# Kernel optimization log

Hardware: AMD Instinct MI355X
Metric: run time of the kernel (lower is better)

Reference implementation:

```python
import jax, jax.numpy as jnp
import numpy as np

N, CIO, L = 16, 512, 384
DIMHEAD, NUMHEAD, MAXEMBED, DIMGROUP = 64, 8, 384, 8
CHID = DIMHEAD * NUMHEAD


def setup_inputs() -> dict:
    key = jax.random.key(0)
    ks = jax.random.split(key, 12)
    s = 0.05
    return {
        "x": jax.random.normal(ks[0], (N, CIO, L), jnp.float32),
        "xorg": jax.random.normal(ks[1], (N, CIO, L), jnp.float32),
        "abspos": jax.random.normal(ks[2], (N, CIO, L), jnp.float32),
        "mask": jnp.zeros((N, L), jnp.float32),
        "norm": jnp.full((N,), 8.0, jnp.float32),
        "qkpos_res": s * jax.random.normal(ks[3], (CIO // DIMGROUP, 1), jnp.float32),
        "qkorg_res": s * jax.random.normal(ks[4], (CIO // DIMGROUP, 1), jnp.float32),
        "vorg_res": s * jax.random.normal(ks[5], (CIO // DIMGROUP, 1), jnp.float32),
        "relpos": s * jax.random.normal(ks[6], (2 * MAXEMBED - 1,), jnp.float32),
        "gate_w": s * jax.random.normal(ks[7], (NUMHEAD, CIO), jnp.float32),
        "gate_b": jnp.zeros((NUMHEAD,), jnp.float32),
        "q_w": s * jax.random.normal(ks[8], (CHID, CIO), jnp.float32),
        "k_w": s * jax.random.normal(ks[9], (CHID, CIO), jnp.float32),
        "v_w": s * jax.random.normal(ks[10], (CHID, CIO), jnp.float32),
        "dense_w": s * jax.random.normal(ks[11], (CIO, CHID), jnp.float32),
        "dense_b": jnp.zeros((CIO,), jnp.float32),
    }


def _rezero(t, res):
    # (N,C,L) -> reshape to (N, C//DIMGROUP, DIMGROUP*L), scale per group, reshape back
    n, c, l = t.shape
    return (t.reshape(n, c // DIMGROUP, -1) * res).reshape(n, c, l)


def _relpos_idx():
    # idx[i, j] = clip(MAXEMBED - i + j, 0, 2*MAXEMBED - 2)
    idx = np.arange(MAXEMBED, MAXEMBED - L, -1)[:, None] + np.arange(L)[None, :]
    return jnp.asarray(np.clip(idx, 0, 2 * MAXEMBED - 2))


def reference(x, xorg, abspos, mask, norm, qkpos_res, qkorg_res, vorg_res,
              relpos, gate_w, gate_b, q_w, k_w, v_w, dense_w, dense_b):
    n = x.shape[0]
    x0 = x + _rezero(xorg, vorg_res)                     # value path
    x1 = x + _rezero(xorg, qkorg_res) + _rezero(abspos, qkpos_res)  # qk path

    q = jnp.einsum('oc,ncl->nol', q_w, x1).reshape(n, NUMHEAD, DIMHEAD, L)
    k = jnp.einsum('oc,ncl->nol', k_w, x1).reshape(n, NUMHEAD, DIMHEAD, L)
    v = jnp.einsum('oc,ncl->nol', v_w, x0).reshape(n, NUMHEAD, DIMHEAD, L)

    scores = jnp.einsum('nhdi,nhdj->nhij', q, k)         # (N, H, L, L)
    gate = jnp.einsum('oc,ncl->nol', gate_w, x) + gate_b[None, :, None]  # (N, H, L)
    scores = (scores + relpos[_relpos_idx()]
              + gate[:, :, None, :]
              + mask[:, None, None, :]) / norm[:, None, None, None]

    attn = jax.nn.softmax(scores, axis=-1)
    out = jnp.einsum('nhij,nhdj->nhdi', attn, v).reshape(n, CHID, L)
    out = jnp.einsum('oc,ncl->nol', dense_w, out) + dense_b[None, :, None]
    return out
```

## Files before the change

kernel.cpp:

```cpp
#include <hip/hip_runtime.h>
#include <hip/hip_bf16.h>

#define N_B   16
#define CIO   512
#define LSEQ  384
#define DH    64
#define NH    8
#define CHID  512
#define ME    384

typedef __hip_bfloat16 bf16;
typedef __attribute__((ext_vector_type(8))) short bf16x8;
typedef __attribute__((ext_vector_type(4))) float f32x4;

#define AS1 __attribute__((address_space(1)))
#define AS3 __attribute__((address_space(3)))

__device__ __forceinline__ unsigned short f2bs(float f) {
    union { bf16 b; unsigned short u; } cv; cv.b = __float2bfloat16(f); return cv.u;
}

__device__ __forceinline__ void gload_lds16(const bf16* g, bf16* l) {
    __builtin_amdgcn_global_load_lds((const AS1 unsigned int*)g,
                                     (AS3 unsigned int*)l, 16, 0, 0);
}

__launch_bounds__(256)
__global__ void prep_kernel(const float* __restrict__ x, const float* __restrict__ xorg,
                            const float* __restrict__ abspos,
                            const float* __restrict__ qkorg, const float* __restrict__ qkpos,
                            const float* __restrict__ vorg,
                            const float* __restrict__ gw,
                            const float* __restrict__ q_w, const float* __restrict__ k_w,
                            const float* __restrict__ v_w, const float* __restrict__ dense_w,
                            bf16* __restrict__ wqb, bf16* __restrict__ wkb,
                            bf16* __restrict__ wvb, bf16* __restrict__ wdb,
                            bf16* __restrict__ x1t, bf16* __restrict__ x0t,
                            float* __restrict__ gpart)
{
    __shared__ bf16 T1[64 * 72], T0[64 * 72];
    __shared__ float Traw[64 * 65];
    __shared__ float gws[NH * 64];
    __shared__ float r0[64], r1[64], r2[64];
    const int tid = threadIdx.x;
    const int cb = blockIdx.x;
    const int c0 = cb * 64;
    const int l0 = blockIdx.y * 64;
    const int n  = blockIdx.z;

    {
        int f = blockIdx.x + 8 * (blockIdx.y + 6 * blockIdx.z);
        if (f < 512) {
            int e = (f * 256 + tid) * 8;
            int which = e >> 18;
            int off = e & ((1 << 18) - 1);
            const float* s = which == 0 ? q_w : which == 1 ? k_w : which == 2 ? v_w : dense_w;
            bf16* d       = which == 0 ? wqb : which == 1 ? wkb : which == 2 ? wvb : wdb;
            float4 f0 = *(const float4*)&s[off];
            float4 f1 = *(const float4*)&s[off + 4];
            unsigned short u[8] = {f2bs(f0.x), f2bs(f0.y), f2bs(f0.z), f2bs(f0.w),
                                   f2bs(f1.x), f2bs(f1.y), f2bs(f1.z), f2bs(f1.w)};
            *(uint4*)&d[off] = *(uint4*)u;
        }
    }

    if (tid < 64) {
        int gidx = (c0 + tid) >> 3;
        r0[tid] = vorg[gidx];
        r1[tid] = qkorg[gidx];
        r2[tid] = qkpos[gidx];
    }
    for (int t = tid; t < NH * 64; t += 256) {
        int h = t >> 6, c = t & 63;
        gws[t] = gw[h * CIO + c0 + c];
    }
    __syncthreads();
    const int l = tid & 63, cs = tid >> 6;
    #pragma unroll
    for (int r = 0; r < 16; r++) {
        int cl = r * 4 + cs;
        size_t gi = ((size_t)n * CIO + c0 + cl) * LSEQ + l0 + l;
        float xv = x[gi], xo = xorg[gi];
        Traw[cl * 65 + l] = xv;
        T0[l * 72 + cl] = __float2bfloat16(xv + r0[cl] * xo);
        T1[l * 72 + cl] = __float2bfloat16(xv + r1[cl] * xo + r2[cl] * abspos[gi]);
    }
    __syncthreads();
    for (int t = tid; t < NH * 64; t += 256) {
        int h = t >> 6, ll = t & 63;
        float s = 0.f;
        #pragma unroll
        for (int c = 0; c < 64; c++) s += gws[h * 64 + c] * Traw[c * 65 + ll];
        gpart[(((size_t)cb * N_B + n) * NH + h) * LSEQ + l0 + ll] = s;
    }
    #pragma unroll
    for (int t = 0; t < 2; t++) {
        int idx = t * 256 + tid;
        int lr = idx >> 3, u = idx & 7;
        size_t go = ((size_t)n * LSEQ + l0 + lr) * CIO + c0 + u * 8;
        *(uint4*)&x1t[go] = *(const uint4*)&T1[lr * 72 + u * 8];
        *(uint4*)&x0t[go] = *(const uint4*)&T0[lr * 72 + u * 8];
    }
}

__launch_bounds__(256)
__global__ void qkv_kernel(const bf16* __restrict__ wall,
                           const bf16* __restrict__ x1t, const bf16* __restrict__ x0t,
                           bf16* __restrict__ qb, bf16* __restrict__ kb,
                           bf16* __restrict__ vb)
{
    __shared__ __align__(16) char smem[17408];
    bf16* As = (bf16*)smem;
    bf16* Bs = (bf16*)(smem + 8192);
    bf16* S  = (bf16*)smem;

    const int tid = threadIdx.x;
    const int lane = tid & 63, w = tid >> 6;
    const int l15 = lane & 15, g = lane >> 4;
    const int Bid = blockIdx.x;
    const int rres = Bid & 7, qq = Bid >> 3;
    const int n = rres + 8 * (qq / 36);
    const int t = qq % 36;
    const int ot = t / 3;
    const int lt = t % 3;
    const int osub = (w & 1) * 64, lsub = (w >> 1) * 64;

    const bf16* Wt = wall + (size_t)(ot * 128) * CIO;
    const bf16* Bt = (ot < 8 ? x1t : x0t) + ((size_t)n * LSEQ + lt * 128) * CIO;

    const int segA = 2 * w, segB = 2 * w + 1;
    const int eA = segA * 512 + lane * 8;
    const int eB = segB * 512 + lane * 8;
    const int rA = eA >> 5, cA = eA & 31;
    const int rB = eB >> 5, cB = eB & 31;

    f32x4 acc[4][4];
    #pragma unroll
    for (int mt = 0; mt < 4; mt++)
        #pragma unroll
        for (int jt = 0; jt < 4; jt++) acc[mt][jt] = f32x4{0.f, 0.f, 0.f, 0.f};

    for (int it = 0; it < 16; ++it) {
        const int k0 = it * 32;
        gload_lds16(Wt + (size_t)rA * CIO + k0 + cA, As + segA * 512);
        gload_lds16(Wt + (size_t)rB * CIO + k0 + cB, As + segB * 512);
        gload_lds16(Bt + (size_t)rA * CIO + k0 + cA, Bs + segA * 512);
        gload_lds16(Bt + (size_t)rB * CIO + k0 + cB, Bs + segB * 512);
        __syncthreads();
        bf16x8 af[4], bfv[4];
        #pragma unroll
        for (int mt = 0; mt < 4; mt++)
            af[mt] = *(const bf16x8*)&As[(osub + mt * 16 + l15) * 32 + 8 * g];
        #pragma unroll
        for (int jt = 0; jt < 4; jt++)
            bfv[jt] = *(const bf16x8*)&Bs[(lsub + jt * 16 + l15) * 32 + 8 * g];
        #pragma unroll
        for (int mt = 0; mt < 4; mt++)
            #pragma unroll
            for (int jt = 0; jt < 4; jt++)
                acc[mt][jt] = __builtin_amdgcn_mfma_f32_16x16x32_bf16(af[mt], bfv[jt], acc[mt][jt], 0, 0, 0);
        __syncthreads();
    }

    if (ot < 8) {
        bf16* dstb = (ot < 4) ? qb : kb;
        const int hbase = 2 * (ot & 3);
        #pragma unroll
        for (int lh = 0; lh < 2; ++lh) {
            if ((w >> 1) == lh) {
                #pragma unroll
                for (int mt = 0; mt < 4; mt++)
                    #pragma unroll
                    for (int jt = 0; jt < 4; jt++)
                        #pragma unroll
                        for (int r = 0; r < 4; r++)
                            S[(jt * 16 + l15) * 136 + osub + mt * 16 + 4 * g + r] =
                                __float2bfloat16(acc[mt][jt][r]);
            }
            __syncthreads();
            #pragma unroll
            for (int t2 = 0; t2 < 4; ++t2) {
                int idx = t2 * 256 + tid;
                int lr = idx >> 4, u = idx & 15;
                int ho = u >> 3, dc = u & 7;
                bf16* dst = dstb + (((size_t)n * NH + hbase + ho) * LSEQ
                                    + lt * 128 + lh * 64 + lr) * DH + dc * 8;
                *(uint4*)dst = *(const uint4*)&S[lr * 136 + u * 8];
            }
            __syncthreads();
        }
    } else {
        const int ob = (ot - 8) * 128;
        #pragma unroll
        for (int oh = 0; oh < 2; ++oh) {
            if ((w & 1) == oh) {
                #pragma unroll
                for (int mt = 0; mt < 4; mt++)
                    #pragma unroll
                    for (int jt = 0; jt < 4; jt++)
                        #pragma unroll
                        for (int r = 0; r < 4; r++)
                            S[(mt * 16 + 4 * g + r) * 136 + lsub + jt * 16 + l15] =
                                __float2bfloat16(acc[mt][jt][r]);
            }
            __syncthreads();
            #pragma unroll
            for (int t2 = 0; t2 < 4; ++t2) {
                int idx = t2 * 256 + tid;
                int orr = idx >> 4, u = idx & 15;
                bf16* dst = vb + ((size_t)(n * CHID + ob + oh * 64 + orr)) * LSEQ
                               + lt * 128 + u * 8;
                *(uint4*)dst = *(const uint4*)&S[orr * 136 + u * 8];
            }
            __syncthreads();
        }
    }
}

__launch_bounds__(256, 3)
__global__ void attn_kernel(const bf16* __restrict__ qt,
                            const bf16* __restrict__ kt,
                            const bf16* __restrict__ v,
                            const float* __restrict__ gpart,
                            const float* __restrict__ gb,
                            const float* __restrict__ mask,
                            const float* __restrict__ norm,
                            const float* __restrict__ relpos,
                            bf16* __restrict__ ctxt)
{
    __shared__ __align__(16) char smem[25600];
    __shared__ float relp_s[2 * ME - 1];
    __shared__ float radd_s[LSEQ];

    bf16* P = (bf16*)smem;
    bf16* O = (bf16*)smem;

    const int tid = threadIdx.x;
    const int Bid = blockIdx.x;
    const int rres = Bid & 7, qq = Bid >> 3;
    const int n = rres + 8 * (qq / 48);
    const int rem = qq % 48;
    const int h = rem / 6;
    const int i0 = (rem % 6) * 64;
    const int lane = tid & 63;
    const int w = tid >> 6;
    const int l15 = lane & 15, g = lane >> 4;
    const int m0 = w * 16;

    const size_t nh = (size_t)n * NH + h;
    const bf16* kt_g = kt + nh * LSEQ * DH;
    const bf16* vg   = v + ((size_t)n * CHID + h * DH) * LSEQ;

    {
        const float gbh = gb[h];
        for (int i = tid; i < LSEQ; i += 256) {
            float s = gbh + mask[(size_t)n * LSEQ + i];
            #pragma unroll
            for (int cb = 0; cb < 8; cb++)
                s += gpart[(((size_t)cb * N_B + n) * NH + h) * LSEQ + i];
            radd_s[i] = s;
        }
    }
    for (int i = tid; i < 2 * ME - 1; i += 256) relp_s[i] = relpos[i];

    const bf16* qrow = qt + (nh * LSEQ + i0 + m0 + l15) * DH;
    bf16x8 a0 = *(const bf16x8*)&qrow[8 * g];
    bf16x8 a1 = *(const bf16x8*)&qrow[8 * g + 32];
    const float inv_norm = 1.0f / norm[n];
    __syncthreads();

    f32x4 acc[24];
    #pragma unroll
    for (int jt = 0; jt < 24; jt++) acc[jt] = f32x4{0.f, 0.f, 0.f, 0.f};
    #pragma unroll
    for (int jt = 0; jt < 24; jt++) {
        const bf16* kr = &kt_g[(size_t)(jt * 16 + l15) * DH + 8 * g];
        bf16x8 b0 = *(const bf16x8*)kr;
        bf16x8 b1 = *(const bf16x8*)(kr + 32);
        acc[jt] = __builtin_amdgcn_mfma_f32_16x16x32_bf16(a0, b0, acc[jt], 0, 0, 0);
        acc[jt] = __builtin_amdgcn_mfma_f32_16x16x32_bf16(a1, b1, acc[jt], 0, 0, 0);
    }

    const int ib = i0 + m0 + 4 * g;
    float mx[4] = {-1e30f, -1e30f, -1e30f, -1e30f};
    #pragma unroll
    for (int jt = 0; jt < 24; jt++) {
        float ra = radd_s[jt * 16 + l15];
        #pragma unroll
        for (int r = 0; r < 4; r++) {
            int idx = ME - (ib + r) + jt * 16 + l15;
            idx = (idx > 2 * ME - 2) ? (2 * ME - 2) : idx;
            float s = (acc[jt][r] + relp_s[idx] + ra) * inv_norm;
            acc[jt][r] = s;
            mx[r] = fmaxf(mx[r], s);
        }
    }
    #pragma unroll
    for (int r = 0; r < 4; r++)
        #pragma unroll
        for (int off = 1; off <= 8; off <<= 1)
            mx[r] = fmaxf(mx[r], __shfl_xor(mx[r], off));
    float sm[4] = {0.f, 0.f, 0.f, 0.f};
    #pragma unroll
    for (int jt = 0; jt < 24; jt++) {
        #pragma unroll
        for (int r = 0; r < 4; r++) {
            float e = __expf(acc[jt][r] - mx[r]);
            acc[jt][r] = e;
            sm[r] += e;
        }
    }
    #pragma unroll
    for (int r = 0; r < 4; r++) {
        #pragma unroll
        for (int off = 1; off <= 8; off <<= 1)
            sm[r] += __shfl_xor(sm[r], off);
        sm[r] = 1.0f / sm[r];
    }

    f32x4 oacc[4];
    #pragma unroll
    for (int dn = 0; dn < 4; dn++) oacc[dn] = f32x4{0.f, 0.f, 0.f, 0.f};
    #pragma unroll
    for (int half = 0; half < 2; half++) {
        #pragma unroll
        for (int jt = 0; jt < 12; jt++)
            #pragma unroll
            for (int r = 0; r < 4; r++)
                P[(m0 + 4 * g + r) * 200 + jt * 16 + l15] =
                    __float2bfloat16(acc[half * 12 + jt][r] * sm[r]);
        bf16x8 vreg[2][4];
        #pragma unroll
        for (int dn = 0; dn < 4; dn++)
            vreg[0][dn] = *(const bf16x8*)&vg[(size_t)(dn * 16 + l15) * LSEQ + half * 192 + 8 * g];
        #pragma unroll
        for (int jt2 = 0; jt2 < 6; jt2++) {
            const int s = jt2 & 1;
            if (jt2 < 5) {
                #pragma unroll
                for (int dn = 0; dn < 4; dn++)
                    vreg[s ^ 1][dn] = *(const bf16x8*)&vg[(size_t)(dn * 16 + l15) * LSEQ + half * 192 + (jt2 + 1) * 32 + 8 * g];
            }
            bf16x8 a = *(const bf16x8*)&P[(m0 + l15) * 200 + jt2 * 32 + 8 * g];
            #pragma unroll
            for (int dn = 0; dn < 4; dn++)
                oacc[dn] = __builtin_amdgcn_mfma_f32_16x16x32_bf16(a, vreg[s][dn], oacc[dn], 0, 0, 0);
        }
    }

    __syncthreads();
    #pragma unroll
    for (int dn = 0; dn < 4; dn++)
        #pragma unroll
        for (int r = 0; r < 4; r++)
            O[(m0 + 4 * g + r) * 72 + dn * 16 + l15] = __float2bfloat16(oacc[dn][r]);
    __syncthreads();

    bf16* cg_ = ctxt + ((size_t)n * LSEQ + i0) * CHID + h * DH;
    #pragma unroll
    for (int t = 0; t < 2; t++) {
        int idx = t * 256 + tid;
        int ir = idx >> 3, u = idx & 7;
        *(uint4*)&cg_[(size_t)ir * CHID + u * 8] = *(const uint4*)&O[ir * 72 + u * 8];
    }
}

__launch_bounds__(256, 6)
__global__ void dense_kernel(const bf16* __restrict__ Wb,
                             const bf16* __restrict__ Bt,
                             const float* __restrict__ bias,
                             float* __restrict__ outf)
{
    __shared__ __align__(16) float S[64 * 68];
    const int tid = threadIdx.x;
    const int lane = tid & 63, w = tid >> 6;
    const int l15 = lane & 15, g = lane >> 4;
    const int Bid = blockIdx.x;
    const int rres = Bid & 7, qq = Bid >> 3;
    const int n = rres + 8 * (qq / 48);
    const int tt = qq % 48;
    const int o0 = (tt / 6) * 64;
    const int l0 = (tt % 6) * 64;

    const bf16* arow = Wb + (size_t)(o0 + l15) * CIO + 8 * g;
    const bf16* brow = Bt + ((size_t)n * LSEQ + l0 + w * 16 + l15) * CIO + 8 * g;

    f32x4 acc[4];
    #pragma unroll
    for (int mt = 0; mt < 4; mt++) acc[mt] = f32x4{0.f, 0.f, 0.f, 0.f};
    #pragma unroll 4
    for (int it = 0; it < 16; it++) {
        const int k0 = it * 32;
        bf16x8 b = *(const bf16x8*)&brow[k0];
        bf16x8 a[4];
        #pragma unroll
        for (int mt = 0; mt < 4; mt++)
            a[mt] = *(const bf16x8*)&arow[(size_t)mt * 16 * CIO + k0];
        #pragma unroll
        for (int mt = 0; mt < 4; mt++)
            acc[mt] = __builtin_amdgcn_mfma_f32_16x16x32_bf16(a[mt], b, acc[mt], 0, 0, 0);
    }

    #pragma unroll
    for (int mt = 0; mt < 4; mt++)
        #pragma unroll
        for (int r = 0; r < 4; r++)
            S[(mt * 16 + 4 * g + r) * 68 + w * 16 + l15] =
                acc[mt][r] + bias[o0 + mt * 16 + 4 * g + r];
    __syncthreads();
    float* og = outf + ((size_t)n * CHID + o0) * LSEQ + l0;
    #pragma unroll
    for (int t = 0; t < 4; t++) {
        int idx = t * 256 + tid;
        int orow = idx >> 4, u = idx & 15;
        *(float4*)&og[(size_t)orow * LSEQ + u * 4] = *(const float4*)&S[orow * 68 + u * 4];
    }
}

extern "C" void kernel_launch(void* const* d_in, const int* in_sizes, int n_in,
                              void* d_out, int out_size, void* d_ws, size_t ws_size,
                              hipStream_t stream)
{
    const float* x       = (const float*)d_in[0];
    const float* xorg    = (const float*)d_in[1];
    const float* abspos  = (const float*)d_in[2];
    const float* mask    = (const float*)d_in[3];
    const float* norm    = (const float*)d_in[4];
    const float* qkpos   = (const float*)d_in[5];
    const float* qkorg   = (const float*)d_in[6];
    const float* vorg    = (const float*)d_in[7];
    const float* relpos  = (const float*)d_in[8];
    const float* gate_w  = (const float*)d_in[9];
    const float* gate_b  = (const float*)d_in[10];
    const float* q_w     = (const float*)d_in[11];
    const float* k_w     = (const float*)d_in[12];
    const float* v_w     = (const float*)d_in[13];
    const float* dense_w = (const float*)d_in[14];
    const float* dense_b = (const float*)d_in[15];
    float* out = (float*)d_out;

    const size_t TEN = (size_t)N_B * CHID * LSEQ * sizeof(bf16);
    const size_t WB  = (size_t)CHID * CIO * sizeof(bf16);
    char* ws = (char*)d_ws;
    bf16*  x1t  = (bf16*)(ws);
    bf16*  x0t  = (bf16*)(ws + TEN);
    bf16*  qb   = (bf16*)(ws + 2 * TEN);
    bf16*  kb   = (bf16*)(ws + 3 * TEN);
    bf16*  vb   = (bf16*)(ws + 4 * TEN);
    bf16*  wqb  = (bf16*)(ws + 5 * TEN);
    bf16*  wkb  = (bf16*)(ws + 5 * TEN + WB);
    bf16*  wvb  = (bf16*)(ws + 5 * TEN + 2 * WB);
    bf16*  wdb  = (bf16*)(ws + 5 * TEN + 3 * WB);
    float* gpart = (float*)(ws + 5 * TEN + 4 * WB);
    bf16*  ctxt = x1t;

    prep_kernel<<<dim3(CIO / 64, LSEQ / 64, N_B), 256, 0, stream>>>(
        x, xorg, abspos, qkorg, qkpos, vorg, gate_w,
        q_w, k_w, v_w, dense_w, wqb, wkb, wvb, wdb, x1t, x0t, gpart);
    qkv_kernel<<<576, 256, 0, stream>>>(wqb, x1t, x0t, qb, kb, vb);
    attn_kernel<<<768, 256, 0, stream>>>(qb, kb, vb, gpart, gate_b,
                                         mask, norm, relpos, ctxt);
    dense_kernel<<<768, 256, 0, stream>>>(wdb, ctxt, dense_b, out);
}
```

Before: 199.4 us.

## Use online softmax over two key halves to cut score register footprint

```diff
diff --git a/kernel.cpp b/kernel.cpp
--- a/kernel.cpp
+++ b/kernel.cpp
@@ -269,77 +269,75 @@
     const float inv_norm = 1.0f / norm[n];
     __syncthreads();
 
-    f32x4 acc[24];
-    #pragma unroll
-    for (int jt = 0; jt < 24; jt++) acc[jt] = f32x4{0.f, 0.f, 0.f, 0.f};
-    #pragma unroll
-    for (int jt = 0; jt < 24; jt++) {
-        const bf16* kr = &kt_g[(size_t)(jt * 16 + l15) * DH + 8 * g];
-        bf16x8 b0 = *(const bf16x8*)kr;
-        bf16x8 b1 = *(const bf16x8*)(kr + 32);
-        acc[jt] = __builtin_amdgcn_mfma_f32_16x16x32_bf16(a0, b0, acc[jt], 0, 0, 0);
-        acc[jt] = __builtin_amdgcn_mfma_f32_16x16x32_bf16(a1, b1, acc[jt], 0, 0, 0);
-    }
-
     const int ib = i0 + m0 + 4 * g;
-    float mx[4] = {-1e30f, -1e30f, -1e30f, -1e30f};
-    #pragma unroll
-    for (int jt = 0; jt < 24; jt++) {
-        float ra = radd_s[jt * 16 + l15];
+    f32x4 oacc[4];
+    #pragma unroll
+    for (int dn = 0; dn < 4; dn++) oacc[dn] = f32x4{0.f, 0.f, 0.f, 0.f};
+    float m_r[4]  = {-1e30f, -1e30f, -1e30f, -1e30f};
+    float lsum[4] = {0.f, 0.f, 0.f, 0.f};
+
+    #pragma unroll
+    for (int half = 0; half < 2; half++) {
+        const int j0 = half * 192;
+
+        f32x4 acc[12];
+        #pragma unroll
+        for (int jt = 0; jt < 12; jt++) acc[jt] = f32x4{0.f, 0.f, 0.f, 0.f};
+        #pragma unroll
+        for (int jt = 0; jt < 12; jt++) {
+            const bf16* kr = &kt_g[(size_t)(j0 + jt * 16 + l15) * DH + 8 * g];
+            bf16x8 b0 = *(const bf16x8*)kr;
+            bf16x8 b1 = *(const bf16x8*)(kr + 32);
+            acc[jt] = __builtin_amdgcn_mfma_f32_16x16x32_bf16(a0, b0, acc[jt], 0, 0, 0);
+            acc[jt] = __builtin_amdgcn_mfma_f32_16x16x32_bf16(a1, b1, acc[jt], 0, 0, 0);
+        }
+
+        float mx[4] = {-1e30f, -1e30f, -1e30f, -1e30f};
+        #pragma unroll
+        for (int jt = 0; jt < 12; jt++) {
+            float ra = radd_s[j0 + jt * 16 + l15];
+            #pragma unroll
+            for (int r = 0; r < 4; r++) {
+                int idx = ME - (ib + r) + j0 + jt * 16 + l15;
+                idx = (idx > 2 * ME - 2) ? (2 * ME - 2) : idx;
+                float s = (acc[jt][r] + relp_s[idx] + ra) * inv_norm;
+                acc[jt][r] = s;
+                mx[r] = fmaxf(mx[r], s);
+            }
+        }
         #pragma unroll
         for (int r = 0; r < 4; r++) {
-            int idx = ME - (ib + r) + jt * 16 + l15;
-            idx = (idx > 2 * ME - 2) ? (2 * ME - 2) : idx;
-            float s = (acc[jt][r] + relp_s[idx] + ra) * inv_norm;
-            acc[jt][r] = s;
-            mx[r] = fmaxf(mx[r], s);
-        }
-    }
-    #pragma unroll
-    for (int r = 0; r < 4; r++)
-        #pragma unroll
-        for (int off = 1; off <= 8; off <<= 1)
-            mx[r] = fmaxf(mx[r], __shfl_xor(mx[r], off));
-    float sm[4] = {0.f, 0.f, 0.f, 0.f};
-    #pragma unroll
-    for (int jt = 0; jt < 24; jt++) {
-        #pragma unroll
-        for (int r = 0; r < 4; r++) {
-            float e = __expf(acc[jt][r] - mx[r]);
-            acc[jt][r] = e;
-            sm[r] += e;
-        }
-    }
-    #pragma unroll
-    for (int r = 0; r < 4; r++) {
-        #pragma unroll
-        for (int off = 1; off <= 8; off <<= 1)
-            sm[r] += __shfl_xor(sm[r], off);
-        sm[r] = 1.0f / sm[r];
-    }
-
-    f32x4 oacc[4];
-    #pragma unroll
-    for (int dn = 0; dn < 4; dn++) oacc[dn] = f32x4{0.f, 0.f, 0.f, 0.f};
-    #pragma unroll
-    for (int half = 0; half < 2; half++) {
-        #pragma unroll
-        for (int jt = 0; jt < 12; jt++)
-            #pragma unroll
-            for (int r = 0; r < 4; r++)
-                P[(m0 + 4 * g + r) * 200 + jt * 16 + l15] =
-                    __float2bfloat16(acc[half * 12 + jt][r] * sm[r]);
+            #pragma unroll
+            for (int off = 1; off <= 8; off <<= 1)
+                mx[r] = fmaxf(mx[r], __shfl_xor(mx[r], off));
+            float mnew = fmaxf(m_r[r], mx[r]);
+            float sc = __expf(m_r[r] - mnew);
+            m_r[r] = mnew;
+            lsum[r] *= sc;
+            #pragma unroll
+            for (int dn = 0; dn < 4; dn++) oacc[dn][r] *= sc;
+        }
+        #pragma unroll
+        for (int jt = 0; jt < 12; jt++) {
+            #pragma unroll
+            for (int r = 0; r < 4; r++) {
+                float e = __expf(acc[jt][r] - m_r[r]);
+                lsum[r] += e;
+                P[(m0 + 4 * g + r) * 200 + jt * 16 + l15] = __float2bfloat16(e);
+            }
+        }
+
         bf16x8 vreg[2][4];
         #pragma unroll
         for (int dn = 0; dn < 4; dn++)
-            vreg[0][dn] = *(const bf16x8*)&vg[(size_t)(dn * 16 + l15) * LSEQ + half * 192 + 8 * g];
+            vreg[0][dn] = *(const bf16x8*)&vg[(size_t)(dn * 16 + l15) * LSEQ + j0 + 8 * g];
         #pragma unroll
         for (int jt2 = 0; jt2 < 6; jt2++) {
             const int s = jt2 & 1;
             if (jt2 < 5) {
                 #pragma unroll
                 for (int dn = 0; dn < 4; dn++)
-                    vreg[s ^ 1][dn] = *(const bf16x8*)&vg[(size_t)(dn * 16 + l15) * LSEQ + half * 192 + (jt2 + 1) * 32 + 8 * g];
+                    vreg[s ^ 1][dn] = *(const bf16x8*)&vg[(size_t)(dn * 16 + l15) * LSEQ + j0 + (jt2 + 1) * 32 + 8 * g];
             }
             bf16x8 a = *(const bf16x8*)&P[(m0 + l15) * 200 + jt2 * 32 + 8 * g];
             #pragma unroll
@@ -348,12 +346,21 @@
         }
     }
 
+    float rs[4];
+    #pragma unroll
+    for (int r = 0; r < 4; r++) {
+        float t = lsum[r];
+        #pragma unroll
+        for (int off = 1; off <= 8; off <<= 1) t += __shfl_xor(t, off);
+        rs[r] = 1.0f / t;
+    }
+
     __syncthreads();
     #pragma unroll
     for (int dn = 0; dn < 4; dn++)
         #pragma unroll
         for (int r = 0; r < 4; r++)
-            O[(m0 + 4 * g + r) * 72 + dn * 16 + l15] = __float2bfloat16(oacc[dn][r]);
+            O[(m0 + 4 * g + r) * 72 + dn * 16 + l15] = __float2bfloat16(oacc[dn][r] * rs[r]);
     __syncthreads();
 
     bf16* cg_ = ctxt + ((size_t)n * LSEQ + i0) * CHID + h * DH;
```

Result: no change. 197.6 us (-0.9%).
